# Optimization experiments

Hardware: AMD Instinct MI355X
Metric: run time of the kernel (lower is better)

The kernel has to match this reference:

```python
import jax, jax.numpy as jnp
import numpy as np

B, S, H = 2, 512, 1024
D = 24            # hdim_proj_dim
MLP_H = 96        # hdim_mlp_hidden
VAL_IN = 2 * H    # concat_only
OUT_HID = 2 * max(128, H // 2)  # 1024


def setup_inputs() -> dict:
    key = jax.random.key(0)
    ks = jax.random.split(key, 12)
    sc = 0.02
    return {
        "H_j": jax.random.normal(ks[0], (B, S, H), jnp.float32),
        "H_i": jax.random.normal(ks[1], (B, S, H), jnp.float32),
        "attn_mask": jnp.ones((B, S), jnp.float32),
        "p_j": jax.random.normal(ks[2], (H, D), jnp.float32) * sc,
        "p_i": jax.random.normal(ks[3], (H, D), jnp.float32) * sc,
        "W1": jax.random.normal(ks[4], (4 * D, MLP_H), jnp.float32) * sc,
        "b1": jnp.zeros((MLP_H,), jnp.float32),
        "W2": jax.random.normal(ks[5], (MLP_H, 1), jnp.float32) * sc,
        "b2": jnp.zeros((1,), jnp.float32),
        "Wv1": jax.random.normal(ks[6], (VAL_IN, OUT_HID), jnp.float32) * sc,
        "bv1": jnp.zeros((OUT_HID,), jnp.float32),
        "Wv2": jax.random.normal(ks[7], (OUT_HID, H), jnp.float32) * sc,
        "bv2": jnp.zeros((H,), jnp.float32),
        "alpha": jnp.asarray(0.05, jnp.float32),
    }


def reference(H_j, H_i, attn_mask, p_j, p_i, W1, b1, W2, b2, Wv1, bv1, Wv2, bv2, alpha):
    # Low-dim projections: [B,S,D]
    Zj = jnp.einsum('bsh,hd->bsd', H_j, p_j)
    Zi = jnp.einsum('bsh,hd->bsd', H_i, p_i)
    # 4-term pairwise features: [B,S,S,4D]
    Zj_b = jnp.broadcast_to(Zj[:, :, None, :], (B, S, S, D))
    Zi_b = jnp.broadcast_to(Zi[:, None, :, :], (B, S, S, D))
    pair = jnp.concatenate([Zj_b, Zi_b, Zj_b * Zi_b, jnp.abs(Zj_b - Zi_b)], axis=-1)
    # Pair-score MLP -> logits [B,S,S]
    h = jax.nn.relu(jnp.einsum('bjif,fm->bjim', pair, W1) + b1)
    logits = (jnp.einsum('bjim,mo->bjio', h, W2) + b2)[..., 0]
    # additive key-side mask (same as torch _expand_mask_last)
    logits = logits + (1.0 - attn_mask)[:, None, :] * jnp.finfo(logits.dtype).min
    # token_temp == 1.0 -> no scaling
    probs = jax.nn.softmax(logits, axis=-1)  # over keys i
    ctx = jnp.einsum('bji,bih->bjh', probs, H_i)  # [B,S,H]
    # Value fusion MLP (concat_only), dropout is identity in eval
    msg_in = jnp.concatenate([ctx, H_j], axis=-1)  # [B,S,2H]
    msg = jax.nn.relu(jnp.einsum('bsf,fo->bso', msg_in, Wv1) + bv1)
    msg = jnp.einsum('bso,oh->bsh', msg, Wv2) + bv2
    return alpha * msg
```

## Files before the change

kernel.cpp:

```cpp
#include <hip/hip_runtime.h>
#include <math.h>

#define B_    2
#define S_    512
#define HDIM  1024
#define D_    24
#define M_    96
#define ROWS  (B_*S_)

typedef _Float16 half8 __attribute__((ext_vector_type(8)));
typedef float    f32x4 __attribute__((ext_vector_type(4)));
typedef unsigned short ushort8 __attribute__((ext_vector_type(8)));

__device__ __forceinline__ void transpose_tile64_cache(
    const float* __restrict__ in, _Float16* __restrict__ out,
    int R, int C, int xt, int yt, int t) {
  int R0 = yt * 64, C0 = xt * 64;
  int c = t >> 2, rq = (t & 3) * 16;
  _Float16 o[16];
  const float* src = in + (size_t)(R0 + rq) * C + C0 + c;
#pragma unroll
  for (int e = 0; e < 16; ++e) o[e] = (_Float16)src[(size_t)e * C];
  _Float16* dst = out + (size_t)(C0 + c) * R + R0 + rq;
  *(ushort8*)dst = *(ushort8*)o;
  *(ushort8*)(dst + 8) = *(ushort8*)&o[8];
}

template <bool EMITH>
__device__ __forceinline__ void proj_mfma64(
    const float* __restrict__ H, const float* __restrict__ P,
    float* __restrict__ Z, _Float16* __restrict__ Himg,
    int r0, char* smem, int t) {
  const int w = t >> 6, l = t & 63;
  const int lo = l & 15, hi = l >> 4;
  const int row = r0 + w * 16 + lo;
  const float* hrow = H + (size_t)row * HDIM;
  f32x4 acc0 = {}, acc1 = {};

  for (int ph = 0; ph < 2; ++ph) {
    if (ph) __syncthreads();
    for (int q = 0; q < 8; ++q) {
      int s = t + q * 256;
      int slo = s & 15, shi = (s >> 4) & 3, snt = (s >> 6) & 1, sst = s >> 7;
      int d = snt * 16 + slo;
      half8 v = {};
      if (d < D_) {
        int k = (ph * 16 + sst) * 32 + shi * 8;
#pragma unroll
        for (int e = 0; e < 8; ++e)
          v[e] = (_Float16)P[(size_t)(k + e) * D_ + d];
      }
      *(half8*)(smem + s * 16) = v;
    }
    __syncthreads();

    for (int st = 0; st < 16; ++st) {
      int step = ph * 16 + st;
      const float* src = hrow + step * 32 + hi * 8;
      float4 v0 = *(const float4*)src;
      float4 v1 = *(const float4*)(src + 4);
      half8 a8;
      a8[0] = (_Float16)v0.x; a8[1] = (_Float16)v0.y;
      a8[2] = (_Float16)v0.z; a8[3] = (_Float16)v0.w;
      a8[4] = (_Float16)v1.x; a8[5] = (_Float16)v1.y;
      a8[6] = (_Float16)v1.z; a8[7] = (_Float16)v1.w;
      if (EMITH)
        *(half8*)(Himg + (size_t)row * HDIM + step * 32 + hi * 8) = a8;
      half8 b0 = *(const half8*)(smem + ((st * 2 + 0) * 64 + l) * 16);
      half8 b1 = *(const half8*)(smem + ((st * 2 + 1) * 64 + l) * 16);
      acc0 = __builtin_amdgcn_mfma_f32_16x16x32_f16(a8, b0, acc0, 0, 0, 0);
      acc1 = __builtin_amdgcn_mfma_f32_16x16x32_f16(a8, b1, acc1, 0, 0, 0);
    }
  }
#pragma unroll
  for (int rg = 0; rg < 4; ++rg) {
    int zr = r0 + w * 16 + hi * 4 + rg;
    Z[(size_t)zr * D_ + lo] = acc0[rg];
    if (lo < 8) Z[(size_t)zr * D_ + 16 + lo] = acc1[rg];
  }
}

__global__ __launch_bounds__(256) void prep_kernel(
    const float* __restrict__ Hj, const float* __restrict__ Hi,
    const float* __restrict__ pj, const float* __restrict__ pi,
    const float* __restrict__ W1, const float* __restrict__ Wv1,
    const float* __restrict__ Wv2,
    _Float16* __restrict__ HjH, _Float16* __restrict__ HiT,
    _Float16* __restrict__ Wv1T, _Float16* __restrict__ Wv2T,
    _Float16* __restrict__ Wimg, float* __restrict__ Zj,
    float* __restrict__ Zi) {
  __shared__ __attribute__((aligned(16))) char smem[32768];
  const int bid = blockIdx.x;
  const int t = threadIdx.x;

  if (bid < 16) {
    proj_mfma64<true>(Hj, pj, Zj, HjH, bid * 64, smem, t);
  } else if (bid < 32) {
    proj_mfma64<false>(Hi, pi, Zi, nullptr, (bid - 16) * 64, smem, t);
  } else if (bid < 36) {
    int c = (bid - 32) * 256 + t;
    half8 v = {};
    if (c < 864) {
      int kc = c / 96, m = c - kc * 96;
#pragma unroll
      for (int e = 0; e < 8; ++e)
        v[e] = (_Float16)W1[(24 + kc * 8 + e) * M_ + m];
    }
    *(half8*)(Wimg + (size_t)c * 8) = v;
  } else if (bid < 292) {
    int id = bid - 36;
    int z = id >> 7, rem = id & 127;
    transpose_tile64_cache(Hi + (size_t)z * S_ * HDIM,
                           HiT + (size_t)z * HDIM * S_,
                           S_, HDIM, rem & 15, rem >> 4, t);
  } else if (bid < 804) {
    int id = bid - 292;
    transpose_tile64_cache(Wv1, Wv1T, 2 * HDIM, HDIM, id & 15, id >> 4, t);
  } else {
    int id = bid - 804;
    transpose_tile64_cache(Wv2, Wv2T, HDIM, HDIM, id & 15, id >> 4, t);
  }
}

#define FOFFB   0
#define LOGOFFB 40960
#define ZJOFFB  (LOGOFFB + 2048)
#define W2OFFB  (ZJOFFB + 96)
#define AJOFFB  (W2OFFB + 384)
#define REDOFFB (AJOFFB + 384)
#define ZCOFFB  (REDOFFB + 32)
#define LDSB    (ZCOFFB + 16)

__global__ __launch_bounds__(256, 3) void pair_fused_kernel(
    const float* __restrict__ Zj, const float* __restrict__ Zi,
    const float* __restrict__ W1, const float* __restrict__ b1,
    const float* __restrict__ W2, const _Float16* __restrict__ Wimg,
    const float* __restrict__ mask, _Float16* __restrict__ probs) {
  __shared__ __attribute__((aligned(16))) char smem[LDSB];
  const int t = threadIdx.x;
  const int w = t >> 6, l = t & 63;
  const int lo = l & 15, hi = l >> 4;
  const int rj = blockIdx.x;
  const int b = rj >> 9;

  float* zjL    = (float*)(smem + ZJOFFB);
  float* W2s    = (float*)(smem + W2OFFB);
  float* ajL    = (float*)(smem + AJOFFB);
  float* logits = (float*)(smem + LOGOFFB);
  float* red    = (float*)(smem + REDOFFB);

  if (t < D_) zjL[t] = Zj[(size_t)rj * D_ + t];
  if (t < M_) {
    W2s[t] = W2[t];
    float aj = b1[t];
#pragma unroll
    for (int d = 0; d < D_; ++d)
      aj = fmaf(Zj[(size_t)rj * D_ + d], W1[d * M_ + t], aj);
    ajL[t] = aj;
  }
  if (t == 0) {
    half8 z = {};
    *(half8*)(smem + ZCOFFB) = z;
  }

  half8 wf[6][3];
#pragma unroll
  for (int mh = 0; mh < 6; ++mh)
#pragma unroll
    for (int ks = 0; ks < 3; ++ks) {
      int kc = ks * 4 + hi;
      half8 v = {};
      if (kc < 10)
        v = *(const half8*)(Wimg + (size_t)(kc * 96 + mh * 16 + lo) * 8);
      wf[mh][ks] = v;
    }

  __syncthreads();

  if (hi == 1) {
#pragma unroll
    for (int mh = 0; mh < 6; ++mh)
      wf[mh][2][0] = (_Float16)ajL[mh * 16 + lo];
  }
  float w2r[6][4];
#pragma unroll
  for (int mh = 0; mh < 6; ++mh)
#pragma unroll
    for (int r = 0; r < 4; ++r) w2r[mh][r] = W2s[mh * 16 + hi * 4 + r];

  for (int p = 0; p < 2; ++p) {
    {
      int i = p * 256 + t;
      const float* zi = Zi + (size_t)(b * S_ + i) * D_;
      float ziv[D_];
#pragma unroll
      for (int q = 0; q < 6; ++q) {
        float4 v = ((const float4*)zi)[q];
        ziv[q * 4 + 0] = v.x; ziv[q * 4 + 1] = v.y;
        ziv[q * 4 + 2] = v.z; ziv[q * 4 + 3] = v.w;
      }
#pragma unroll
      for (int kc = 0; kc < 3; ++kc) {
        half8 v;
#pragma unroll
        for (int e = 0; e < 8; ++e) v[e] = (_Float16)ziv[kc * 8 + e];
        *(half8*)(smem + FOFFB + (kc * 256 + t) * 16) = v;
      }
#pragma unroll
      for (int kc = 0; kc < 3; ++kc) {
        half8 v;
#pragma unroll
        for (int e = 0; e < 8; ++e) {
          int d = kc * 8 + e;
          v[e] = (_Float16)(zjL[d] * ziv[d]);
        }
        *(half8*)(smem + FOFFB + ((kc + 3) * 256 + t) * 16) = v;
      }
#pragma unroll
      for (int kc = 0; kc < 3; ++kc) {
        half8 v;
#pragma unroll
        for (int e = 0; e < 8; ++e) {
          int d = kc * 8 + e;
          v[e] = (_Float16)fabsf(zjL[d] - ziv[d]);
        }
        *(half8*)(smem + FOFFB + ((kc + 6) * 256 + t) * 16) = v;
      }
      if (p == 0) {
        half8 v = {};
        v[0] = (_Float16)1.0f;
        *(half8*)(smem + FOFFB + (9 * 256 + t) * 16) = v;
      }
    }
    __syncthreads();

#pragma unroll
    for (int nt = 0; nt < 4; ++nt) {
      half8 ff[3];
#pragma unroll
      for (int ks = 0; ks < 3; ++ks) {
        int kc = ks * 4 + hi;
        int off = (kc < 10) ? (FOFFB + (kc * 256 + w * 64 + nt * 16 + lo) * 16) : ZCOFFB;
        ff[ks] = *(const half8*)(smem + off);
      }
      f32x4 a6[6] = {};
      __builtin_amdgcn_s_setprio(1);
#pragma unroll
      for (int ks = 0; ks < 3; ++ks)
#pragma unroll
        for (int mh = 0; mh < 6; ++mh)
          a6[mh] = __builtin_amdgcn_mfma_f32_16x16x32_f16(wf[mh][ks], ff[ks], a6[mh], 0, 0, 0);
      __builtin_amdgcn_s_setprio(0);
      float part = 0.f;
#pragma unroll
      for (int mh = 0; mh < 6; ++mh)
#pragma unroll
        for (int r = 0; r < 4; ++r)
          part = fmaf(fmaxf(a6[mh][r], 0.f), w2r[mh][r], part);
      part += __shfl_xor(part, 16);
      part += __shfl_xor(part, 32);
      if (hi == 0) logits[p * 256 + w * 64 + nt * 16 + lo] = part;
    }
    __syncthreads();
  }

  float m1 = mask[b * S_ + t], m2 = mask[b * S_ + t + 256];
  float lg1 = logits[t]       + (1.0f - m1) * (-3.40282347e38f);
  float lg2 = logits[t + 256] + (1.0f - m2) * (-3.40282347e38f);
  float mx = fmaxf(lg1, lg2);
#pragma unroll
  for (int off = 32; off > 0; off >>= 1) mx = fmaxf(mx, __shfl_xor(mx, off));
  if (l == 0) red[w] = mx;
  __syncthreads();
  float rmax = fmaxf(fmaxf(red[0], red[1]), fmaxf(red[2], red[3]));
  float e1 = __expf(lg1 - rmax);
  float e2 = __expf(lg2 - rmax);
  float s = e1 + e2;
#pragma unroll
  for (int off = 32; off > 0; off >>= 1) s += __shfl_xor(s, off);
  if (l == 0) red[4 + w] = s;
  __syncthreads();
  float inv = 1.0f / (red[4] + red[5] + red[6] + red[7]);
  probs[(size_t)rj * S_ + t]       = (_Float16)(e1 * inv);
  probs[(size_t)rj * S_ + t + 256] = (_Float16)(e2 * inv);
}

template <bool SWZ, bool HASA1, bool RELU, bool FINAL, bool OUTH>
__global__ __launch_bounds__(512) void mfma_gemm_kernel(
    const _Float16* __restrict__ A0, const _Float16* __restrict__ A1,
    const _Float16* __restrict__ Bt, const float* __restrict__ bias,
    const float* __restrict__ alpha_ptr, void* __restrict__ Cout,
    int M, int N, int K0, int K1,
    long aB0, long aB1, long bB, long cB) {
  __shared__ __attribute__((aligned(16))) char smem[65536];
  const int t = threadIdx.x;
  const int w = t >> 6, l = t & 63;
  const int g = w >> 2, wq = w & 3;
  const int K = K0 + K1;
  const int KH = K >> 1;
  const int NT = KH >> 5;
  int n0, m0, zb;
  if (SWZ) {
    int s = (blockIdx.x & 7) * 32 + (blockIdx.x >> 3);
    n0 = (s & 15) * 64; m0 = (s >> 4) * 64; zb = 0;
  } else {
    n0 = blockIdx.x * 64; m0 = blockIdx.y * 64; zb = blockIdx.z;
  }
  const _Float16* A0b = A0 + (size_t)zb * aB0;
  const _Float16* A1b = HASA1 ? (A1 + (size_t)zb * aB1) : nullptr;
  const _Float16* Btb = Bt + (size_t)zb * bB;
  char* gls = smem + (g << 15);

  const int sr = (wq << 4) + (l >> 2);
  const int sk = ((l & 3) ^ ((l >> 3) & 3)) << 3;

  const int mq = wq >> 1, nq = wq & 1;
  int offA[2], offB[2];
#pragma unroll
  for (int i = 0; i < 2; ++i) {
    int ra = mq * 32 + i * 16 + (l & 15);
    offA[i] = ra * 64 + (((l >> 4) ^ ((ra >> 1) & 3)) << 4);
    int rb = nq * 32 + i * 16 + (l & 15);
    offB[i] = 4096 + rb * 64 + (((l >> 4) ^ ((rb >> 1) & 3)) << 4);
  }

  f32x4 acc[2][2] = {};

  auto stage = [&](int tt) {
    char* buf = gls + (tt & 3) * 8192;
    int kg = g * KH + (tt << 5) + sk;
    const _Float16* ga;
    if (HASA1 && kg >= K0) ga = A1b + (size_t)(m0 + sr) * K1 + (kg - K0);
    else                   ga = A0b + (size_t)(m0 + sr) * K0 + kg;
    __builtin_amdgcn_global_load_lds(
        (const __attribute__((address_space(1))) void*)ga,
        (__attribute__((address_space(3))) void*)(buf + (wq << 10)), 16, 0, 0);
    const _Float16* gb = Btb + (size_t)(n0 + sr) * K + kg;
    __builtin_amdgcn_global_load_lds(
        (const __attribute__((address_space(1))) void*)gb,
        (__attribute__((address_space(3))) void*)(buf + 4096 + (wq << 10)), 16, 0, 0);
  };

  stage(0);
  stage(1);
  stage(2);

  for (int tt = 0; tt < NT; ++tt) {
    if (tt + 2 < NT)      asm volatile("s_waitcnt vmcnt(4)" ::: "memory");
    else if (tt + 1 < NT) asm volatile("s_waitcnt vmcnt(2)" ::: "memory");
    else                  asm volatile("s_waitcnt vmcnt(0)" ::: "memory");
    __builtin_amdgcn_s_barrier();
    __builtin_amdgcn_sched_barrier(0);
    const char* buf = gls + (tt & 3) * 8192;
    half8 a0 = *(const half8*)(buf + offA[0]);
    half8 a1 = *(const half8*)(buf + offA[1]);
    half8 b0 = *(const half8*)(buf + offB[0]);
    half8 b1v = *(const half8*)(buf + offB[1]);
    acc[0][0] = __builtin_amdgcn_mfma_f32_16x16x32_f16(a0, b0, acc[0][0], 0, 0, 0);
    acc[0][1] = __builtin_amdgcn_mfma_f32_16x16x32_f16(a0, b1v, acc[0][1], 0, 0, 0);
    acc[1][0] = __builtin_amdgcn_mfma_f32_16x16x32_f16(a1, b0, acc[1][0], 0, 0, 0);
    acc[1][1] = __builtin_amdgcn_mfma_f32_16x16x32_f16(a1, b1v, acc[1][1], 0, 0, 0);
    if (tt + 3 < NT) stage(tt + 3);
  }

  const int lr = l & 15, lq = l >> 4;
  float* redm = (float*)smem;
  __syncthreads();
  if (g == 1) {
#pragma unroll
    for (int mi = 0; mi < 2; ++mi)
#pragma unroll
      for (int ni = 0; ni < 2; ++ni)
#pragma unroll
        for (int rg = 0; rg < 4; ++rg)
          redm[(mq * 32 + mi * 16 + lq * 4 + rg) * 68 + nq * 32 + ni * 16 + lr] =
              acc[mi][ni][rg];
  }
  __syncthreads();
  if (g == 0) {
    const float alpha = FINAL ? *alpha_ptr : 1.0f;
    const size_t cbase = (size_t)zb * cB;
#pragma unroll
    for (int mi = 0; mi < 2; ++mi)
#pragma unroll
      for (int ni = 0; ni < 2; ++ni) {
        int col = n0 + nq * 32 + ni * 16 + lr;
        float bv = bias ? bias[col] : 0.0f;
#pragma unroll
        for (int rg = 0; rg < 4; ++rg) {
          int row = m0 + mq * 32 + mi * 16 + lq * 4 + rg;
          float x = acc[mi][ni][rg] +
                    redm[(mq * 32 + mi * 16 + lq * 4 + rg) * 68 + nq * 32 + ni * 16 + lr] +
                    bv;
          if (RELU) x = fmaxf(x, 0.f);
          if (FINAL) x *= alpha;
          if (OUTH)
            ((_Float16*)Cout)[cbase + (size_t)row * N + col] = (_Float16)x;
          else
            ((float*)Cout)[cbase + (size_t)row * N + col] = x;
        }
      }
  }
}

extern "C" void kernel_launch(void* const* d_in, const int* in_sizes, int n_in,
                              void* d_out, int out_size, void* d_ws, size_t ws_size,
                              hipStream_t stream) {
  const float* Hj   = (const float*)d_in[0];
  const float* Hi   = (const float*)d_in[1];
  const float* mask = (const float*)d_in[2];
  const float* pj   = (const float*)d_in[3];
  const float* pi   = (const float*)d_in[4];
  const float* W1   = (const float*)d_in[5];
  const float* b1   = (const float*)d_in[6];
  const float* W2   = (const float*)d_in[7];
  const float* Wv1  = (const float*)d_in[9];
  const float* bv1  = (const float*)d_in[10];
  const float* Wv2  = (const float*)d_in[11];
  const float* bv2  = (const float*)d_in[12];
  const float* alpha = (const float*)d_in[13];

  char* w = (char*)d_ws;
  float* Zj  = (float*)w;            w += (size_t)ROWS * D_ * 4;
  float* Zi  = (float*)w;            w += (size_t)ROWS * D_ * 4;
  _Float16* Wimg   = (_Float16*)w;   w += (size_t)1024 * 16;
  _Float16* probsH = (_Float16*)w;   w += (size_t)B_ * S_ * S_ * 2;
  _Float16* HjH    = (_Float16*)w;   w += (size_t)ROWS * HDIM * 2;
  _Float16* HiT    = (_Float16*)w;   w += (size_t)B_ * HDIM * S_ * 2;
  _Float16* Wv1T   = (_Float16*)w;   w += (size_t)HDIM * 2 * HDIM * 2;
  _Float16* Wv2T   = (_Float16*)w;   w += (size_t)HDIM * HDIM * 2;
  _Float16* ctxH   = (_Float16*)w;   w += (size_t)ROWS * HDIM * 2;
  _Float16* hidH   = (_Float16*)w;   w += (size_t)ROWS * HDIM * 2;
  float* out = (float*)d_out;

  prep_kernel<<<1060, 256, 0, stream>>>(Hj, Hi, pj, pi, W1, Wv1, Wv2,
                                        HjH, HiT, Wv1T, Wv2T, Wimg, Zj, Zi);

  pair_fused_kernel<<<ROWS, 256, 0, stream>>>(Zj, Zi, W1, b1, W2, Wimg,
                                              mask, probsH);

  mfma_gemm_kernel<false, false, false, false, true><<<dim3(16, 8, 2), 512, 0, stream>>>(
      probsH, nullptr, HiT, nullptr, nullptr, ctxH,
      S_, HDIM, S_, 0, (long)S_ * S_, 0, (long)HDIM * S_, (long)S_ * HDIM);
  mfma_gemm_kernel<true, true, true, false, true><<<dim3(256), 512, 0, stream>>>(
      ctxH, HjH, Wv1T, bv1, nullptr, hidH,
      ROWS, HDIM, HDIM, HDIM, 0, 0, 0, 0);
  mfma_gemm_kernel<true, false, false, true, false><<<dim3(256), 512, 0, stream>>>(
      hidH, nullptr, Wv2T, bv2, alpha, out,
      ROWS, HDIM, HDIM, 0, 0, 0, 0, 0);
}
```

Measured before the change: 69.01 us.

## Reassociate ctx@Wv1a as probs@(Hi@Wv1a) and merge into pair kernel

Rather than materialising ctx = probs@Hi and then multiplying by the ctx half of Wv1, the code precomputes GT = (Hi@Wv1a)^T per batch, in extra blocks of the pair-score kernel. The first value-MLP GEMM then becomes probs@GT + Hj@Wv1b in a single kernel with K = 512+1024, which drops one GEMM launch and the ctx round-trip. The Hi transpose is replaced by a plain fp16 copy emitted during projection. The FLOPs are roughly unchanged, and GT is rounded to fp16 before the probs multiply, which changes the rounding behaviour slightly.

```diff
diff --git a/kernel.cpp b/kernel.cpp
--- a/kernel.cpp
+++ b/kernel.cpp
@@ -26,7 +26,6 @@
   *(ushort8*)(dst + 8) = *(ushort8*)&o[8];
 }
 
-template <bool EMITH>
 __device__ __forceinline__ void proj_mfma64(
     const float* __restrict__ H, const float* __restrict__ P,
     float* __restrict__ Z, _Float16* __restrict__ Himg,
@@ -64,8 +63,7 @@
       a8[2] = (_Float16)v0.z; a8[3] = (_Float16)v0.w;
       a8[4] = (_Float16)v1.x; a8[5] = (_Float16)v1.y;
       a8[6] = (_Float16)v1.z; a8[7] = (_Float16)v1.w;
-      if (EMITH)
-        *(half8*)(Himg + (size_t)row * HDIM + step * 32 + hi * 8) = a8;
+      *(half8*)(Himg + (size_t)row * HDIM + step * 32 + hi * 8) = a8;
       half8 b0 = *(const half8*)(smem + ((st * 2 + 0) * 64 + l) * 16);
       half8 b1 = *(const half8*)(smem + ((st * 2 + 1) * 64 + l) * 16);
       acc0 = __builtin_amdgcn_mfma_f32_16x16x32_f16(a8, b0, acc0, 0, 0, 0);
@@ -85,18 +83,18 @@
     const float* __restrict__ pj, const float* __restrict__ pi,
     const float* __restrict__ W1, const float* __restrict__ Wv1,
     const float* __restrict__ Wv2,
-    _Float16* __restrict__ HjH, _Float16* __restrict__ HiT,
-    _Float16* __restrict__ Wv1T, _Float16* __restrict__ Wv2T,
-    _Float16* __restrict__ Wimg, float* __restrict__ Zj,
-    float* __restrict__ Zi) {
+    _Float16* __restrict__ HjH, _Float16* __restrict__ HiH,
+    _Float16* __restrict__ Wv1aT, _Float16* __restrict__ Wv1bT,
+    _Float16* __restrict__ Wv2T, _Float16* __restrict__ Wimg,
+    float* __restrict__ Zj, float* __restrict__ Zi) {
   __shared__ __attribute__((aligned(16))) char smem[32768];
   const int bid = blockIdx.x;
   const int t = threadIdx.x;
 
   if (bid < 16) {
-    proj_mfma64<true>(Hj, pj, Zj, HjH, bid * 64, smem, t);
+    proj_mfma64(Hj, pj, Zj, HjH, bid * 64, smem, t);
   } else if (bid < 32) {
-    proj_mfma64<false>(Hi, pi, Zi, nullptr, (bid - 16) * 64, smem, t);
+    proj_mfma64(Hi, pi, Zi, HiH, (bid - 16) * 64, smem, t);
   } else if (bid < 36) {
     int c = (bid - 32) * 256 + t;
     half8 v = {};
@@ -109,15 +107,13 @@
     *(half8*)(Wimg + (size_t)c * 8) = v;
   } else if (bid < 292) {
     int id = bid - 36;
-    int z = id >> 7, rem = id & 127;
-    transpose_tile64_cache(Hi + (size_t)z * S_ * HDIM,
-                           HiT + (size_t)z * HDIM * S_,
-                           S_, HDIM, rem & 15, rem >> 4, t);
-  } else if (bid < 804) {
+    transpose_tile64_cache(Wv1, Wv1aT, HDIM, HDIM, id & 15, id >> 4, t);
+  } else if (bid < 548) {
     int id = bid - 292;
-    transpose_tile64_cache(Wv1, Wv1T, 2 * HDIM, HDIM, id & 15, id >> 4, t);
+    transpose_tile64_cache(Wv1 + (size_t)HDIM * HDIM, Wv1bT, HDIM, HDIM,
+                           id & 15, id >> 4, t);
   } else {
-    int id = bid - 804;
+    int id = bid - 548;
     transpose_tile64_cache(Wv2, Wv2T, HDIM, HDIM, id & 15, id >> 4, t);
   }
 }
@@ -131,18 +127,86 @@
 #define ZCOFFB  (REDOFFB + 32)
 #define LDSB    (ZCOFFB + 16)
 
-__global__ __launch_bounds__(256, 3) void pair_fused_kernel(
+__global__ __launch_bounds__(256, 3) void pair_gt_kernel(
     const float* __restrict__ Zj, const float* __restrict__ Zi,
     const float* __restrict__ W1, const float* __restrict__ b1,
     const float* __restrict__ W2, const _Float16* __restrict__ Wimg,
-    const float* __restrict__ mask, _Float16* __restrict__ probs) {
+    const float* __restrict__ mask, _Float16* __restrict__ probs,
+    const _Float16* __restrict__ Wv1aT, const _Float16* __restrict__ HiH,
+    _Float16* __restrict__ GT) {
   __shared__ __attribute__((aligned(16))) char smem[LDSB];
   const int t = threadIdx.x;
   const int w = t >> 6, l = t & 63;
   const int lo = l & 15, hi = l >> 4;
+
+  if (blockIdx.x >= ROWS) {
+    int id = blockIdx.x - ROWS;
+    int zb = id >> 7, rem = id & 127;
+    int n0 = (rem & 7) * 64, m0 = (rem >> 3) * 64;
+    const _Float16* Bb = HiH + (size_t)zb * S_ * HDIM;
+    _Float16* GTb = GT + (size_t)zb * HDIM * S_;
+
+    const int sr = (w << 4) + (l >> 2);
+    const int sk = ((l & 3) ^ ((l >> 3) & 3)) << 3;
+    const int mq = w >> 1, nq = w & 1;
+    int offA[2], offB[2];
+#pragma unroll
+    for (int i = 0; i < 2; ++i) {
+      int ra = mq * 32 + i * 16 + (l & 15);
+      offA[i] = ra * 64 + (((l >> 4) ^ ((ra >> 1) & 3)) << 4);
+      int rb = nq * 32 + i * 16 + (l & 15);
+      offB[i] = 4096 + rb * 64 + (((l >> 4) ^ ((rb >> 1) & 3)) << 4);
+    }
+    f32x4 acc[2][2] = {};
+
+    auto stage = [&](int tt) {
+      char* buf = smem + (tt & 3) * 8192;
+      int kg = (tt << 5) + sk;
+      const _Float16* ga = Wv1aT + (size_t)(m0 + sr) * HDIM + kg;
+      __builtin_amdgcn_global_load_lds(
+          (const __attribute__((address_space(1))) void*)ga,
+          (__attribute__((address_space(3))) void*)(buf + (w << 10)), 16, 0, 0);
+      const _Float16* gb = Bb + (size_t)(n0 + sr) * HDIM + kg;
+      __builtin_amdgcn_global_load_lds(
+          (const __attribute__((address_space(1))) void*)gb,
+          (__attribute__((address_space(3))) void*)(buf + 4096 + (w << 10)), 16, 0, 0);
+    };
+    stage(0); stage(1); stage(2);
+    const int NT = HDIM >> 5;
+    for (int tt = 0; tt < NT; ++tt) {
+      if (tt + 2 < NT)      asm volatile("s_waitcnt vmcnt(4)" ::: "memory");
+      else if (tt + 1 < NT) asm volatile("s_waitcnt vmcnt(2)" ::: "memory");
+      else                  asm volatile("s_waitcnt vmcnt(0)" ::: "memory");
+      __builtin_amdgcn_s_barrier();
+      __builtin_amdgcn_sched_barrier(0);
+      const char* buf = smem + (tt & 3) * 8192;
+      half8 a0 = *(const half8*)(buf + offA[0]);
+      half8 a1 = *(const half8*)(buf + offA[1]);
+      half8 b0 = *(const half8*)(buf + offB[0]);
+      half8 b1v = *(const half8*)(buf + offB[1]);
+      acc[0][0] = __builtin_amdgcn_mfma_f32_16x16x32_f16(a0, b0, acc[0][0], 0, 0, 0);
+      acc[0][1] = __builtin_amdgcn_mfma_f32_16x16x32_f16(a0, b1v, acc[0][1], 0, 0, 0);
+      acc[1][0] = __builtin_amdgcn_mfma_f32_16x16x32_f16(a1, b0, acc[1][0], 0, 0, 0);
+      acc[1][1] = __builtin_amdgcn_mfma_f32_16x16x32_f16(a1, b1v, acc[1][1], 0, 0, 0);
+      if (tt + 3 < NT) stage(tt + 3);
+    }
+    const int lr = l & 15, lq = l >> 4;
+#pragma unroll
+    for (int mi = 0; mi < 2; ++mi)
+#pragma unroll
+      for (int ni = 0; ni < 2; ++ni) {
+        int col = n0 + nq * 32 + ni * 16 + lr;
+#pragma unroll
+        for (int rg = 0; rg < 4; ++rg) {
+          int row = m0 + mq * 32 + mi * 16 + lq * 4 + rg;
+          GTb[(size_t)row * S_ + col] = (_Float16)acc[mi][ni][rg];
+        }
+      }
+    return;
+  }
+
   const int rj = blockIdx.x;
   const int b = rj >> 9;
-
   float* zjL    = (float*)(smem + ZJOFFB);
   float* W2s    = (float*)(smem + W2OFFB);
   float* ajL    = (float*)(smem + AJOFFB);
@@ -285,13 +349,13 @@
   probs[(size_t)rj * S_ + t + 256] = (_Float16)(e2 * inv);
 }
 
-template <bool SWZ, bool HASA1, bool RELU, bool FINAL, bool OUTH>
+template <bool SWZ, bool HASA1, bool HASB1, bool RELU, bool FINAL, bool OUTH>
 __global__ __launch_bounds__(512) void mfma_gemm_kernel(
     const _Float16* __restrict__ A0, const _Float16* __restrict__ A1,
-    const _Float16* __restrict__ Bt, const float* __restrict__ bias,
-    const float* __restrict__ alpha_ptr, void* __restrict__ Cout,
-    int M, int N, int K0, int K1,
-    long aB0, long aB1, long bB, long cB) {
+    const _Float16* __restrict__ B0, const _Float16* __restrict__ B1,
+    const float* __restrict__ bias, const float* __restrict__ alpha_ptr,
+    void* __restrict__ Cout, int M, int N, int K0, int K1,
+    long aB0, long aB1, long bB0, long cB) {
   __shared__ __attribute__((aligned(16))) char smem[65536];
   const int t = threadIdx.x;
   const int w = t >> 6, l = t & 63;
@@ -308,7 +372,8 @@
   }
   const _Float16* A0b = A0 + (size_t)zb * aB0;
   const _Float16* A1b = HASA1 ? (A1 + (size_t)zb * aB1) : nullptr;
-  const _Float16* Btb = Bt + (size_t)zb * bB;
+  const _Float16* B0b = B0 + (size_t)zb * bB0;
+  const int ldB0 = HASB1 ? K0 : K;
   char* gls = smem + (g << 15);
 
   const int sr = (wq << 4) + (l >> 2);
@@ -335,7 +400,9 @@
     __builtin_amdgcn_global_load_lds(
         (const __attribute__((address_space(1))) void*)ga,
         (__attribute__((address_space(3))) void*)(buf + (wq << 10)), 16, 0, 0);
-    const _Float16* gb = Btb + (size_t)(n0 + sr) * K + kg;
+    const _Float16* gb;
+    if (HASB1 && kg >= K0) gb = B1 + (size_t)(n0 + sr) * K1 + (kg - K0);
+    else                   gb = B0b + (size_t)(n0 + sr) * ldB0 + kg;
     __builtin_amdgcn_global_load_lds(
         (const __attribute__((address_space(1))) void*)gb,
         (__attribute__((address_space(3))) void*)(buf + 4096 + (wq << 10)), 16, 0, 0);
@@ -426,26 +493,29 @@
   _Float16* Wimg   = (_Float16*)w;   w += (size_t)1024 * 16;
   _Float16* probsH = (_Float16*)w;   w += (size_t)B_ * S_ * S_ * 2;
   _Float16* HjH    = (_Float16*)w;   w += (size_t)ROWS * HDIM * 2;
-  _Float16* HiT    = (_Float16*)w;   w += (size_t)B_ * HDIM * S_ * 2;
-  _Float16* Wv1T   = (_Float16*)w;   w += (size_t)HDIM * 2 * HDIM * 2;
+  _Float16* HiH    = (_Float16*)w;   w += (size_t)ROWS * HDIM * 2;
+  _Float16* Wv1aT  = (_Float16*)w;   w += (size_t)HDIM * HDIM * 2;
+  _Float16* Wv1bT  = (_Float16*)w;   w += (size_t)HDIM * HDIM * 2;
   _Float16* Wv2T   = (_Float16*)w;   w += (size_t)HDIM * HDIM * 2;
-  _Float16* ctxH   = (_Float16*)w;   w += (size_t)ROWS * HDIM * 2;
+  _Float16* GT     = (_Float16*)w;   w += (size_t)B_ * HDIM * S_ * 2;
   _Float16* hidH   = (_Float16*)w;   w += (size_t)ROWS * HDIM * 2;
   float* out = (float*)d_out;
 
-  prep_kernel<<<1060, 256, 0, stream>>>(Hj, Hi, pj, pi, W1, Wv1, Wv2,
-                                        HjH, HiT, Wv1T, Wv2T, Wimg, Zj, Zi);
-
-  pair_fused_kernel<<<ROWS, 256, 0, stream>>>(Zj, Zi, W1, b1, W2, Wimg,
-                                              mask, probsH);
-
-  mfma_gemm_kernel<false, false, false, false, true><<<dim3(16, 8, 2), 512, 0, stream>>>(
-      probsH, nullptr, HiT, nullptr, nullptr, ctxH,
-      S_, HDIM, S_, 0, (long)S_ * S_, 0, (long)HDIM * S_, (long)S_ * HDIM);
-  mfma_gemm_kernel<true, true, true, false, true><<<dim3(256), 512, 0, stream>>>(
-      ctxH, HjH, Wv1T, bv1, nullptr, hidH,
-      ROWS, HDIM, HDIM, HDIM, 0, 0, 0, 0);
-  mfma_gemm_kernel<true, false, false, true, false><<<dim3(256), 512, 0, stream>>>(
-      hidH, nullptr, Wv2T, bv2, alpha, out,
+  prep_kernel<<<804, 256, 0, stream>>>(Hj, Hi, pj, pi, W1, Wv1, Wv2,
+                                       HjH, HiH, Wv1aT, Wv1bT, Wv2T, Wimg,
+                                       Zj, Zi);
+
+  pair_gt_kernel<<<ROWS + 256, 256, 0, stream>>>(Zj, Zi, W1, b1, W2, Wimg,
+                                                 mask, probsH, Wv1aT, HiH, GT);
+
+  mfma_gemm_kernel<false, true, true, true, false, true>
+      <<<dim3(16, 8, 2), 512, 0, stream>>>(
+      probsH, HjH, GT, Wv1bT, bv1, nullptr, hidH,
+      S_, HDIM, S_, HDIM,
+      (long)S_ * S_, (long)S_ * HDIM, (long)HDIM * S_, (long)S_ * HDIM);
+
+  mfma_gemm_kernel<true, false, false, false, true, false>
+      <<<dim3(256), 512, 0, stream>>>(
+      hidH, nullptr, Wv2T, nullptr, bv2, alpha, out,
       ROWS, HDIM, HDIM, 0, 0, 0, 0, 0);
 }
```

Result: faster. 65.01 us, median of 2 (-5.8%).
